# Optimization experiments

Hardware: AMD Instinct MI355X
Metric: run time of the kernel (lower is better)

Reference implementation:

```python
import jax, jax.numpy as jnp
import numpy as np
from functools import partial

NUM_QUERIES = 900
TOPK_PRE = 100      # topk(100) in source
TOPK_POST = 20      # keep_inds[:20] in source
IOU_THR = 0.7


def cxcywh_to_xyxy(b):
    cx, cy, w, h = b[..., 0], b[..., 1], b[..., 2], b[..., 3]
    return jnp.stack([cx - 0.5 * w, cy - 0.5 * h, cx + 0.5 * w, cy + 0.5 * h], axis=-1)


def nms_single(boxes, scores):
    # boxes: [K,4] xyxy, already sorted by descending score (top_k output).
    # Single class per patch in this module, so batched_nms == plain nms.
    K = boxes.shape[0]
    area = jnp.clip(boxes[:, 2] - boxes[:, 0], 0) * jnp.clip(boxes[:, 3] - boxes[:, 1], 0)
    lt = jnp.maximum(boxes[:, None, :2], boxes[None, :, :2])
    rb = jnp.minimum(boxes[:, None, 2:], boxes[None, :, 2:])
    wh = jnp.clip(rb - lt, 0)
    inter = wh[..., 0] * wh[..., 1]
    iou = inter / (area[:, None] + area[None, :] - inter + 1e-7)  # [K,K]
    idx = jnp.arange(K)

    def body(i, keep):
        sup = (iou[i] > IOU_THR) & (idx > i) & keep[i]
        return keep & (~sup)

    keep = jax.lax.fori_loop(0, K, body, jnp.ones((K,), bool))
    rank = jnp.cumsum(keep) - 1
    valid = keep & (rank < TOPK_POST)
    slot = jnp.where(valid, rank, TOPK_POST)  # invalid entries scatter into dropped slot
    sel_s = jnp.zeros((TOPK_POST + 1,), scores.dtype).at[slot].set(jnp.where(valid, scores, 0.0))[:TOPK_POST]
    sel_b = jnp.zeros((TOPK_POST + 1, 4), boxes.dtype).at[slot].set(jnp.where(valid[:, None], boxes, 0.0))[:TOPK_POST]
    vmask = jnp.zeros((TOPK_POST + 1,), bool).at[slot].set(valid)[:TOPK_POST]
    return sel_s, sel_b, vmask


def setup_inputs() -> dict:
    key = jax.random.key(0)
    k1, k2, k3, k4 = jax.random.split(key, 4)
    BS, P, Q, C = 16, 64, NUM_QUERIES, 2
    pred_logits = jax.random.normal(k1, (BS, 1, P * Q, C), jnp.float32)
    pred_boxes = jax.random.uniform(k2, (BS, 1, P * Q, 4), jnp.float32, minval=0.05, maxval=0.6)
    target_sizes = jax.random.uniform(k3, (BS, 2), jnp.float32, minval=480.0, maxval=1333.0)  # (h, w)
    labels = jax.random.randint(k4, (BS, P), 0, 80, jnp.int32)
    return {"pred_logits": pred_logits, "pred_boxes": pred_boxes,
            "target_sizes": target_sizes, "labels": labels}


def reference(pred_logits, pred_boxes, target_sizes, labels):
    BS = pred_logits.shape[0]
    Q = NUM_QUERIES
    score = jax.nn.sigmoid(pred_logits[:, 0, :, -1])          # [BS, N]
    boxes = cxcywh_to_xyxy(pred_boxes[:, 0])                   # [BS, N, 4]
    img_h, img_w = target_sizes[:, 0], target_sizes[:, 1]
    scale = jnp.stack([img_w, img_h, img_w, img_h], axis=-1)   # [BS, 4]
    boxes = boxes * scale[:, None, :]
    P = score.shape[1] // Q
    score = score.reshape(BS, P, Q)
    boxes = boxes.reshape(BS, P, Q, 4)
    top_s, top_i = jax.lax.top_k(score, TOPK_PRE)              # [BS, P, 100]
    top_b = jnp.take_along_axis(boxes, top_i[..., None], axis=2)  # [BS, P, 100, 4]
    sel_s, sel_b, vmask = jax.vmap(nms_single)(
        top_b.reshape(BS * P, TOPK_PRE, 4), top_s.reshape(BS * P, TOPK_PRE))
    sel_s = sel_s.reshape(BS, P, TOPK_POST)
    sel_b = sel_b.reshape(BS, P, TOPK_POST, 4)
    vmask = vmask.reshape(BS, P, TOPK_POST)
    sel_l = jnp.where(vmask, labels[:, :, None], -1)
    return sel_s, sel_b, sel_l, vmask
```

## Files before the change

kernel.cpp:

```cpp
#include <hip/hip_runtime.h>
#include <stdint.h>

#define NQ 900
#define TOPK_PRE 100
#define TOPK_POST 20
#define IOU_THR 0.7f
#define THREADS 256

typedef unsigned long long u64;


__global__ __launch_bounds__(THREADS)
void ovnms_kernel(const float* __restrict__ logits,
                  const float* __restrict__ boxes,
                  const float* __restrict__ tsize,
                  const int*   __restrict__ labels,
                  float* __restrict__ out)
{
#pragma clang fp contract(off)
    const int row = blockIdx.x;
    const int b   = row >> 6;
    const int p   = row & 63;
    const int tid = threadIdx.x;
    const int lane = tid & 63;
    const int wid  = tid >> 6;

    __shared__ int hist[256];
    __shared__ u64 sel[128];
    __shared__ u64 sortk[128];
    __shared__ u64 sup0[TOPK_PRE], sup1[TOPK_PRE];
    __shared__ float x1s[TOPK_PRE], y1s[TOPK_PRE], x2s[TOPK_PRE], y2s[TOPK_PRE];
    __shared__ float areas[TOPK_PRE], scs[TOPK_PRE];
    __shared__ int   slots[TOPK_POST];
    __shared__ int   nkeep, sh_cnt, sh_rn, sh_done;
    __shared__ u64   sh_prefix, sh_pivot;

    const float* lrow = logits + ((size_t)b * 57600 + (size_t)p * NQ) * 2;
    u64 kreg[4];
#pragma unroll
    for (int t = 0; t < 4; ++t) {
        int q = tid + t * THREADS;
        u64 key = ~0ull;
        if (q < NQ) {
            float x = lrow[q * 2 + 1];
            float s = 1.0f / (1.0f + expf(-x));
            unsigned u = __float_as_uint(s);
            key = ((u64)(~u) << 32) | (unsigned)q;
        }
        kreg[t] = key;
    }

    if (tid == 0) { sh_prefix = 0; sh_rn = TOPK_PRE; sh_done = 0; sh_pivot = ~0ull; }

    for (int d = 7; d >= 0; --d) {
        __syncthreads();
        if (sh_done) break;
        hist[tid] = 0;
        __syncthreads();
        const int sh1 = 8 * d + 8;
        const u64 pref = sh_prefix;
        const int rn = sh_rn;
#pragma unroll
        for (int t = 0; t < 4; ++t) {
            u64 k = kreg[t];
            bool match = (sh1 >= 64) || ((k >> sh1) == pref);
            if (match) atomicAdd(&hist[(int)((k >> (8 * d)) & 0xFF)], 1);
        }
        __syncthreads();
        if (tid < 64) {
            int c0 = hist[tid * 4 + 0], c1 = hist[tid * 4 + 1];
            int c2 = hist[tid * 4 + 2], c3 = hist[tid * 4 + 3];
            int s = c0 + c1 + c2 + c3;
            int inc = s;
            for (int off = 1; off < 64; off <<= 1) {
                int v = __shfl_up(inc, off);
                if (tid >= off) inc += v;
            }
            int exc = inc - s;
            bool mine = (rn > exc) && (rn <= inc);
            int B = 0, cumB = 0, cntB = 0;
            if (mine) {
                int cum = exc;
                int cc[4] = {c0, c1, c2, c3};
#pragma unroll
                for (int t = 0; t < 4; ++t) {
                    if (rn > cum && rn <= cum + cc[t]) { B = tid * 4 + t; cumB = cum; cntB = cc[t]; }
                    cum += cc[t];
                }
            }
            u64 bal = __ballot(mine);
            int src = __ffsll((unsigned long long)bal) - 1;
            B    = __shfl(B, src);
            cumB = __shfl(cumB, src);
            cntB = __shfl(cntB, src);
            if (tid == 0) {
                int nrn = rn - cumB;
                u64 npref = (pref << 8) | (unsigned)B;
                sh_prefix = npref;
                sh_rn = nrn;
                if (nrn == cntB) {
                    sh_done = 1;
                    sh_pivot = ((npref + 1) << (8 * d)) - 1;
                }
            }
        }
    }

    if (tid < 128) sel[tid] = ~0ull;
    if (tid == 0) sh_cnt = 0;
    __syncthreads();
    const u64 P = sh_pivot;
#pragma unroll
    for (int t = 0; t < 4; ++t) {
        u64 k = kreg[t];
        if (k <= P) { int pos = atomicAdd(&sh_cnt, 1); sel[pos] = k; }
    }
    __syncthreads();

    if (tid < 64) {
        u64 va = sel[tid], vb = sel[tid + 64];
        for (int k = 2; k <= 128; k <<= 1) {
            for (int j = k >> 1; j; j >>= 1) {
                if (j == 64) {
                    bool up = ((tid & k) == 0);
                    u64 lo = va < vb ? va : vb;
                    u64 hi = va < vb ? vb : va;
                    va = up ? lo : hi;
                    vb = up ? hi : lo;
                } else {
                    u64 pa = __shfl_xor(va, j);
                    u64 pb = __shfl_xor(vb, j);
                    bool lower = ((tid & j) == 0);
                    bool dirA = ((tid & k) == 0);
                    bool dirB = (((tid + 64) & k) == 0);
                    va = (dirA == lower) ? (va < pa ? va : pa) : (va > pa ? va : pa);
                    vb = (dirB == lower) ? (vb < pb ? vb : pb) : (vb > pb ? vb : pb);
                }
            }
        }
        sortk[tid] = va;
        sortk[tid + 64] = vb;
    }
    __syncthreads();

    if (tid < TOPK_PRE) {
        u64 key = sortk[tid];
        int q = (int)(key & 0xFFFFFFFFu);
        scs[tid] = __uint_as_float(~(unsigned)(key >> 32));
        const float* brow = boxes + ((size_t)b * 57600 + (size_t)p * NQ + (size_t)q) * 4;
        float cx = brow[0], cy = brow[1], w = brow[2], h = brow[3];
        float ih = tsize[b * 2 + 0];
        float iw = tsize[b * 2 + 1];
        float xa = (cx - 0.5f * w) * iw;
        float ya = (cy - 0.5f * h) * ih;
        float xb = (cx + 0.5f * w) * iw;
        float yb = (cy + 0.5f * h) * ih;
        x1s[tid] = xa; y1s[tid] = ya; x2s[tid] = xb; y2s[tid] = yb;
        areas[tid] = fmaxf(xb - xa, 0.0f) * fmaxf(yb - ya, 0.0f);
    }
    __syncthreads();

    for (int i = wid; i < TOPK_PRE; i += 4) {
        float xi1 = x1s[i], yi1 = y1s[i], xi2 = x2s[i], yi2 = y2s[i], ai = areas[i];
        int j = lane;
        bool b0 = false;
        if (j < i) {
            float ltx = fmaxf(xi1, x1s[j]);
            float lty = fmaxf(yi1, y1s[j]);
            float rbx = fminf(xi2, x2s[j]);
            float rby = fminf(yi2, y2s[j]);
            float wx = fmaxf(rbx - ltx, 0.0f);
            float wy = fmaxf(rby - lty, 0.0f);
            float inter = wx * wy;
            float iou = inter / (((ai + areas[j]) - inter) + 1e-7f);
            b0 = iou > IOU_THR;
        }
        u64 m0 = __ballot(b0);
        j = 64 + lane;
        bool b1 = false;
        if (j < i) {
            float ltx = fmaxf(xi1, x1s[j]);
            float lty = fmaxf(yi1, y1s[j]);
            float rbx = fminf(xi2, x2s[j]);
            float rby = fminf(yi2, y2s[j]);
            float wx = fmaxf(rbx - ltx, 0.0f);
            float wy = fmaxf(rby - lty, 0.0f);
            float inter = wx * wy;
            float iou = inter / (((ai + areas[j]) - inter) + 1e-7f);
            b1 = iou > IOU_THR;
        }
        u64 m1 = __ballot(b1);
        if (lane == 0) { sup0[i] = m0; sup1[i] = m1; }
    }
    __syncthreads();

    if (tid == 0) {
        u64 kept0 = 0, kept1 = 0;
        int r = 0;
#pragma unroll 10
        for (int i = 0; i < TOPK_PRE; ++i) {
            u64 s0 = sup0[i] & kept0;
            u64 s1 = sup1[i] & kept1;
            if ((s0 | s1) == 0ull) {
                if (i < 64) kept0 |= 1ull << i;
                else        kept1 |= 1ull << (i - 64);
                if (r < TOPK_POST) slots[r] = i;
                r++;
            }
        }
        nkeep = r < TOPK_POST ? r : TOPK_POST;
    }
    __syncthreads();

    if (tid < TOPK_POST) {
        size_t o = (size_t)row * TOPK_POST + (size_t)tid;
        float s = 0.0f, xa = 0.0f, ya = 0.0f, xb = 0.0f, yb = 0.0f;
        float lab = -1.0f, m = 0.0f;
        if (tid < nkeep) {
            int i = slots[tid];
            s = scs[i];
            xa = x1s[i]; ya = y1s[i]; xb = x2s[i]; yb = y2s[i];
            lab = (float)labels[row];
            m = 1.0f;
        }
        out[o] = s;
        float* ob = out + 20480 + o * 4;
        ob[0] = xa; ob[1] = ya; ob[2] = xb; ob[3] = yb;
        out[102400 + o] = lab;
        out[122880 + o] = m;
    }
}

extern "C" void kernel_launch(void* const* d_in, const int* in_sizes, int n_in,
                              void* d_out, int out_size, void* d_ws, size_t ws_size,
                              hipStream_t stream) {
    const float* logits = (const float*)d_in[0];
    const float* boxes  = (const float*)d_in[1];
    const float* tsize  = (const float*)d_in[2];
    const int*   labels = (const int*)d_in[3];
    float* out = (float*)d_out;

    ovnms_kernel<<<dim3(1024), dim3(THREADS), 0, stream>>>(logits, boxes, tsize, labels, out);
}
```

Measured before the change: 38.27 us.

## Replace radix-select top-k with per-wave bitonic sort and merge tree

The multi-pass radix select (histogram with shared atomics and several block barriers per digit) followed by a 128-element bitonic sort is replaced. Each wave now bitonic-sorts its 256 keys in registers using shuffles. Two rounds of bitonic top-128 merges through shared memory then produce the sorted top-128. This removes most block-wide barriers and atomic traffic, at the cost of more shuffle and compare work per thread.

```diff
diff --git a/kernel.cpp b/kernel.cpp
--- a/kernel.cpp
+++ b/kernel.cpp
@@ -8,6 +8,9 @@
 #define THREADS 256
 
 typedef unsigned long long u64;
+
+__device__ __forceinline__ u64 umin64(u64 a, u64 b) { return a < b ? a : b; }
+__device__ __forceinline__ u64 umax64(u64 a, u64 b) { return a > b ? a : b; }
 
 
 __global__ __launch_bounds__(THREADS)
@@ -18,133 +21,112 @@
                   float* __restrict__ out)
 {
 #pragma clang fp contract(off)
-    const int row = blockIdx.x;
-    const int b   = row >> 6;
-    const int p   = row & 63;
-    const int tid = threadIdx.x;
+    const int row  = blockIdx.x;
+    const int b    = row >> 6;
+    const int p    = row & 63;
+    const int tid  = threadIdx.x;
     const int lane = tid & 63;
     const int wid  = tid >> 6;
 
-    __shared__ int hist[256];
-    __shared__ u64 sel[128];
-    __shared__ u64 sortk[128];
+    __shared__ u64 wl[4 * 128];
+    __shared__ u64 md[2 * 128];
+    __shared__ u64 fin[128];
     __shared__ u64 sup0[TOPK_PRE], sup1[TOPK_PRE];
     __shared__ float x1s[TOPK_PRE], y1s[TOPK_PRE], x2s[TOPK_PRE], y2s[TOPK_PRE];
     __shared__ float areas[TOPK_PRE], scs[TOPK_PRE];
     __shared__ int   slots[TOPK_POST];
-    __shared__ int   nkeep, sh_cnt, sh_rn, sh_done;
-    __shared__ u64   sh_prefix, sh_pivot;
-
-    const float* lrow = logits + ((size_t)b * 57600 + (size_t)p * NQ) * 2;
-    u64 kreg[4];
-#pragma unroll
-    for (int t = 0; t < 4; ++t) {
-        int q = tid + t * THREADS;
+    __shared__ int   nkeep;
+
+    const float2* l2 = (const float2*)(logits + ((size_t)b * 57600 + (size_t)p * NQ) * 2);
+    u64 kr[4];
+#pragma unroll
+    for (int r = 0; r < 4; ++r) {
+        int q = wid * 64 + lane + r * 256;
         u64 key = ~0ull;
         if (q < NQ) {
-            float x = lrow[q * 2 + 1];
+            float x = l2[q].y;
             float s = 1.0f / (1.0f + expf(-x));
             unsigned u = __float_as_uint(s);
             key = ((u64)(~u) << 32) | (unsigned)q;
         }
-        kreg[t] = key;
-    }
-
-    if (tid == 0) { sh_prefix = 0; sh_rn = TOPK_PRE; sh_done = 0; sh_pivot = ~0ull; }
-
-    for (int d = 7; d >= 0; --d) {
-        __syncthreads();
-        if (sh_done) break;
-        hist[tid] = 0;
-        __syncthreads();
-        const int sh1 = 8 * d + 8;
-        const u64 pref = sh_prefix;
-        const int rn = sh_rn;
-#pragma unroll
-        for (int t = 0; t < 4; ++t) {
-            u64 k = kreg[t];
-            bool match = (sh1 >= 64) || ((k >> sh1) == pref);
-            if (match) atomicAdd(&hist[(int)((k >> (8 * d)) & 0xFF)], 1);
-        }
-        __syncthreads();
-        if (tid < 64) {
-            int c0 = hist[tid * 4 + 0], c1 = hist[tid * 4 + 1];
-            int c2 = hist[tid * 4 + 2], c3 = hist[tid * 4 + 3];
-            int s = c0 + c1 + c2 + c3;
-            int inc = s;
-            for (int off = 1; off < 64; off <<= 1) {
-                int v = __shfl_up(inc, off);
-                if (tid >= off) inc += v;
-            }
-            int exc = inc - s;
-            bool mine = (rn > exc) && (rn <= inc);
-            int B = 0, cumB = 0, cntB = 0;
-            if (mine) {
-                int cum = exc;
-                int cc[4] = {c0, c1, c2, c3};
-#pragma unroll
-                for (int t = 0; t < 4; ++t) {
-                    if (rn > cum && rn <= cum + cc[t]) { B = tid * 4 + t; cumB = cum; cntB = cc[t]; }
-                    cum += cc[t];
+        kr[r] = key;
+    }
+
+#pragma unroll
+    for (int k = 2; k <= 256; k <<= 1) {
+#pragma unroll
+        for (int j = k >> 1; j > 0; j >>= 1) {
+            if (j >= 64) {
+                const int jr = j >> 6;
+#pragma unroll
+                for (int r = 0; r < 4; ++r) {
+                    if ((r & jr) == 0) {
+                        const int rp = r | jr;
+                        bool up = (((r * 64) & k) == 0);
+                        u64 lo = umin64(kr[r], kr[rp]);
+                        u64 hi = umax64(kr[r], kr[rp]);
+                        kr[r]  = up ? lo : hi;
+                        kr[rp] = up ? hi : lo;
+                    }
+                }
+            } else {
+#pragma unroll
+                for (int r = 0; r < 4; ++r) {
+                    bool up = (((r * 64 + lane) & k) == 0);
+                    u64 part = __shfl_xor(kr[r], j);
+                    bool lower = ((lane & j) == 0);
+                    kr[r] = (up == lower) ? umin64(kr[r], part) : umax64(kr[r], part);
                 }
             }
-            u64 bal = __ballot(mine);
-            int src = __ffsll((unsigned long long)bal) - 1;
-            B    = __shfl(B, src);
-            cumB = __shfl(cumB, src);
-            cntB = __shfl(cntB, src);
-            if (tid == 0) {
-                int nrn = rn - cumB;
-                u64 npref = (pref << 8) | (unsigned)B;
-                sh_prefix = npref;
-                sh_rn = nrn;
-                if (nrn == cntB) {
-                    sh_done = 1;
-                    sh_pivot = ((npref + 1) << (8 * d)) - 1;
-                }
-            }
-        }
-    }
-
-    if (tid < 128) sel[tid] = ~0ull;
-    if (tid == 0) sh_cnt = 0;
-    __syncthreads();
-    const u64 P = sh_pivot;
-#pragma unroll
-    for (int t = 0; t < 4; ++t) {
-        u64 k = kreg[t];
-        if (k <= P) { int pos = atomicAdd(&sh_cnt, 1); sel[pos] = k; }
-    }
-    __syncthreads();
-
-    if (tid < 64) {
-        u64 va = sel[tid], vb = sel[tid + 64];
-        for (int k = 2; k <= 128; k <<= 1) {
-            for (int j = k >> 1; j; j >>= 1) {
-                if (j == 64) {
-                    bool up = ((tid & k) == 0);
-                    u64 lo = va < vb ? va : vb;
-                    u64 hi = va < vb ? vb : va;
-                    va = up ? lo : hi;
-                    vb = up ? hi : lo;
-                } else {
-                    u64 pa = __shfl_xor(va, j);
-                    u64 pb = __shfl_xor(vb, j);
-                    bool lower = ((tid & j) == 0);
-                    bool dirA = ((tid & k) == 0);
-                    bool dirB = (((tid + 64) & k) == 0);
-                    va = (dirA == lower) ? (va < pa ? va : pa) : (va > pa ? va : pa);
-                    vb = (dirB == lower) ? (vb < pb ? vb : pb) : (vb > pb ? vb : pb);
-                }
-            }
-        }
-        sortk[tid] = va;
-        sortk[tid + 64] = vb;
+        }
+    }
+
+    wl[wid * 128 + lane]      = kr[0];
+    wl[wid * 128 + 64 + lane] = kr[1];
+    __syncthreads();
+
+    if (wid < 2) {
+        const u64* A = &wl[(2 * wid) * 128];
+        const u64* B = &wl[(2 * wid + 1) * 128];
+        u64 c0 = umin64(A[lane],      B[127 - lane]);
+        u64 c1 = umin64(A[64 + lane], B[63 - lane]);
+        u64 lo = umin64(c0, c1), hi = umax64(c0, c1);
+        c0 = lo; c1 = hi;
+#pragma unroll
+        for (int j = 32; j > 0; j >>= 1) {
+            bool lower = (lane & j) == 0;
+            u64 p0 = __shfl_xor(c0, j);
+            u64 p1 = __shfl_xor(c1, j);
+            c0 = lower ? umin64(c0, p0) : umax64(c0, p0);
+            c1 = lower ? umin64(c1, p1) : umax64(c1, p1);
+        }
+        md[wid * 128 + lane]      = c0;
+        md[wid * 128 + 64 + lane] = c1;
+    }
+    __syncthreads();
+
+    if (wid == 0) {
+        const u64* A = md;
+        const u64* B = md + 128;
+        u64 c0 = umin64(A[lane],      B[127 - lane]);
+        u64 c1 = umin64(A[64 + lane], B[63 - lane]);
+        u64 lo = umin64(c0, c1), hi = umax64(c0, c1);
+        c0 = lo; c1 = hi;
+#pragma unroll
+        for (int j = 32; j > 0; j >>= 1) {
+            bool lower = (lane & j) == 0;
+            u64 p0 = __shfl_xor(c0, j);
+            u64 p1 = __shfl_xor(c1, j);
+            c0 = lower ? umin64(c0, p0) : umax64(c0, p0);
+            c1 = lower ? umin64(c1, p1) : umax64(c1, p1);
+        }
+        fin[lane]      = c0;
+        fin[64 + lane] = c1;
     }
     __syncthreads();
 
     if (tid < TOPK_PRE) {
-        u64 key = sortk[tid];
+        u64 key = fin[tid];
         int q = (int)(key & 0xFFFFFFFFu);
         scs[tid] = __uint_as_float(~(unsigned)(key >> 32));
         const float* brow = boxes + ((size_t)b * 57600 + (size_t)p * NQ + (size_t)q) * 4;
```

Result: slower. 42.33 us (+10.6%).
